# Kernel tuning notes

Measured on AMD Instinct MI355X. Metric: run time of the kernel, lower is better.

The kernel has to match this reference:

```python
import jax, jax.numpy as jnp
import numpy as np

G = 128            # grid_size (hardcoded in NeRFRenderer.__init__)
T = 32             # time_size (reduced from 64 to keep working set < 4GB)
CAS = 1            # cascade = 1 + ceil(log2(bound)), bound = 1
DECAY = 0.95
DENSITY_SCALE = 1.0
DENSITY_THRESH = 0.01


def _expand_bits(v):
    # instant-ngp style 10-bit -> 30-bit expansion (works for 7-bit coords of G=128)
    v = (v * jnp.uint32(0x00010001)) & jnp.uint32(0xFF0000FF)
    v = (v * jnp.uint32(0x00000101)) & jnp.uint32(0x0F00F00F)
    v = (v * jnp.uint32(0x00000011)) & jnp.uint32(0xC30C30C3)
    v = (v * jnp.uint32(0x00000005)) & jnp.uint32(0x49249249)
    return v


def _morton3d(coords):
    # coords: [N, 3] int32 in [0, G)
    x = _expand_bits(coords[:, 0].astype(jnp.uint32))
    y = _expand_bits(coords[:, 1].astype(jnp.uint32))
    z = _expand_bits(coords[:, 2].astype(jnp.uint32))
    return (x | (y << 1) | (z << 2)).astype(jnp.int32)


def setup_inputs() -> dict:
    key = jax.random.key(0)
    k1, k2 = jax.random.split(key)
    density_grid = jax.random.normal(k1, (T, CAS, G ** 3), dtype=jnp.float32) * 0.5
    sigmas = jax.random.uniform(k2, (T, CAS, G ** 3), dtype=jnp.float32)
    return {"density_grid": density_grid, "sigmas": sigmas}


def reference(density_grid, sigmas):
    # full-grid branch of update_extra_state (iter_density < 16)
    g = jnp.arange(G, dtype=jnp.int32)
    xx, yy, zz = jnp.meshgrid(g, g, g, indexing='ij')
    coords = jnp.stack([xx.ravel(), yy.ravel(), zz.ravel()], axis=-1)  # [G^3, 3]
    indices = _morton3d(coords)                                        # [G^3]

    # tmp_grid = -1; tmp_grid[t, cas, indices] = sigmas * density_scale
    tmp_grid = -jnp.ones_like(density_grid)
    tmp_grid = tmp_grid.at[:, :, indices].set(sigmas * DENSITY_SCALE)

    # decay / max merge on mutually-valid cells
    valid = (density_grid >= 0) & (tmp_grid >= 0)
    new_grid = jnp.where(valid, jnp.maximum(density_grid * DECAY, tmp_grid), density_grid)

    # threshold + packbits into bitfield (8 cells per byte, morton order)
    mean_density = jnp.mean(jnp.clip(new_grid, 0.0))
    thresh = jnp.minimum(mean_density, jnp.float32(DENSITY_THRESH))
    bits = (new_grid > thresh).reshape(T, -1, 8)                       # [T, CAS*G^3/8, 8]
    weights = (jnp.int32(1) << jnp.arange(8, dtype=jnp.int32))
    bitfield = jnp.sum(bits.astype(jnp.int32) * weights, axis=-1)      # [T, CAS*G^3/8]
    return new_grid, bitfield
```

## Files before the change

### kernel.cpp

```cpp
#include <hip/hip_runtime.h>

#define G    128
#define G3   (G * G * G)
#define TDIM 32
#define NTOT (TDIM * G3)
#define NBYTES_OUT (NTOT / 8)
#define DECAY 0.95f
#define DTH   0.01f
#define NBLK  (TDIM * 256)

typedef float f32x4 __attribute__((ext_vector_type(4)));
typedef float f32x2 __attribute__((ext_vector_type(2)));

__device__ __forceinline__ unsigned expand3(unsigned v) {
    v = (v * 0x00010001u) & 0xFF0000FFu;
    v = (v * 0x00000101u) & 0x0F00F00Fu;
    v = (v * 0x00000011u) & 0xC30C30C3u;
    v = (v * 0x00000005u) & 0x49249249u;
    return v;
}

__device__ __forceinline__ int swz(int f) {
    return f ^ ((((f >> 11) & 1) << 2) | (((f >> 8) & 1) << 3) | (((f >> 12) & 1) << 4));
}

__device__ __forceinline__ f32x4 merge4(f32x4 v, f32x4 s) {
    f32x4 r;
    r.x = (v.x >= 0.f && s.x >= 0.f) ? fmaxf(v.x * DECAY, s.x) : v.x;
    r.y = (v.y >= 0.f && s.y >= 0.f) ? fmaxf(v.y * DECAY, s.y) : v.y;
    r.z = (v.z >= 0.f && s.z >= 0.f) ? fmaxf(v.z * DECAY, s.z) : v.z;
    r.w = (v.w >= 0.f && s.w >= 0.f) ? fmaxf(v.w * DECAY, s.w) : v.w;
    return r;
}

__global__ __launch_bounds__(512, 8) void
pass1(const float* __restrict__ dg, const float* __restrict__ sg,
      float* __restrict__ out_grid, float* __restrict__ out_bits,
      float* __restrict__ sum_acc)
{
    __shared__ float smem[8192];
    __shared__ float wsum[8];
    const int blk  = blockIdx.x;
    const int t    = blk >> 8;
    const int pp   = blk & 255;
    const int sx   = pp & 15;
    const int sy   = pp >> 4;
    const int base = t * G3;
    const int tid  = threadIdx.x;
    const int w    = tid >> 6;
    const int i    = tid & 63;

    const float* __restrict__ sgt = sg + base + (sx << 17) + (sy << 10);
    f32x4 sa0, sa1, sa2, sa3;
    {
        const int rem = (tid & 255) << 2;
        sa0 = __builtin_nontemporal_load(
                reinterpret_cast<const f32x4*>(sgt + ((tid >> 8) << 14)          + rem));
        sa1 = __builtin_nontemporal_load(
                reinterpret_cast<const f32x4*>(sgt + (((tid + 512) >> 8) << 14)  + rem));
        sa2 = __builtin_nontemporal_load(
                reinterpret_cast<const f32x4*>(sgt + (((tid + 1024) >> 8) << 14) + rem));
        sa3 = __builtin_nontemporal_load(
                reinterpret_cast<const f32x4*>(sgt + (((tid + 1536) >> 8) << 14) + rem));
    }

    const int m_fixed = (int)((expand3((unsigned)sx) << 9) | (expand3((unsigned)sy) << 10));
    const int jgA = base + m_fixed + ((int)expand3((unsigned)w) << 14) + (i << 2);
    const f32x4* dgp = reinterpret_cast<const f32x4*>(dg + jgA);
    const f32x4 v0 = dgp[0];
    const f32x4 v1 = dgp[64];
    const f32x4 v2 = dgp[512];
    const f32x4 v3 = dgp[576];

    {
        const int rem = (tid & 255) << 2;
        *reinterpret_cast<f32x4*>(&smem[swz(((tid >> 8) << 10)          + rem)]) = sa0;
        *reinterpret_cast<f32x4*>(&smem[swz((((tid + 512) >> 8) << 10)  + rem)]) = sa1;
        *reinterpret_cast<f32x4*>(&smem[swz((((tid + 1024) >> 8) << 10) + rem)]) = sa2;
        *reinterpret_cast<f32x4*>(&smem[swz((((tid + 1536) >> 8) << 10) + rem)]) = sa3;
    }
    __syncthreads();

    const int fi = (i & 1) | (((i >> 3) & 1) << 1) | (((i >> 2) & 1) << 8)
                 | (((i >> 5) & 1) << 9) | (((i >> 1) & 1) << 11) | (((i >> 4) & 1) << 12);
    const int S  = (((fi >> 11) & 1) << 2) | (((fi >> 8) & 1) << 3) | (((fi >> 12) & 1) << 4);
    const int A  = w << 4;
    const float* sp0 = &smem[fi | ((A + 0)  ^ S)];
    const float* sp1 = &smem[fi | ((A + 4)  ^ S)];
    const float* sp2 = &smem[fi | ((A + 8)  ^ S)];
    const float* sp3 = &smem[fi | ((A + 12) ^ S)];
    f32x4 s0; s0.x = sp0[0]; s0.y = sp0[1024]; s0.z = sp0[128]; s0.w = sp0[1152];
    f32x4 s1; s1.x = sp1[0]; s1.y = sp1[1024]; s1.z = sp1[128]; s1.w = sp1[1152];
    f32x4 s2; s2.x = sp2[0]; s2.y = sp2[1024]; s2.z = sp2[128]; s2.w = sp2[1152];
    f32x4 s3; s3.x = sp3[0]; s3.y = sp3[1024]; s3.z = sp3[128]; s3.w = sp3[1152];

    const f32x4 r0 = merge4(v0, s0);
    const f32x4 r1 = merge4(v1, s1);
    const f32x4 r2 = merge4(v2, s2);
    const f32x4 r3 = merge4(v3, s3);

    f32x4* ogp = reinterpret_cast<f32x4*>(out_grid + jgA);
    ogp[0]   = r0;
    ogp[64]  = r1;
    ogp[512] = r2;
    ogp[576] = r3;

    float lsum = fmaxf(r0.x, 0.f) + fmaxf(r0.y, 0.f) + fmaxf(r0.z, 0.f) + fmaxf(r0.w, 0.f)
               + fmaxf(r1.x, 0.f) + fmaxf(r1.y, 0.f) + fmaxf(r1.z, 0.f) + fmaxf(r1.w, 0.f)
               + fmaxf(r2.x, 0.f) + fmaxf(r2.y, 0.f) + fmaxf(r2.z, 0.f) + fmaxf(r2.w, 0.f)
               + fmaxf(r3.x, 0.f) + fmaxf(r3.y, 0.f) + fmaxf(r3.z, 0.f) + fmaxf(r3.w, 0.f);

    int n0 = (r0.x > DTH ? 1 : 0) | (r0.y > DTH ? 2 : 0) | (r0.z > DTH ? 4 : 0) | (r0.w > DTH ? 8 : 0);
    int n1 = (r1.x > DTH ? 1 : 0) | (r1.y > DTH ? 2 : 0) | (r1.z > DTH ? 4 : 0) | (r1.w > DTH ? 8 : 0);
    int n2 = (r2.x > DTH ? 1 : 0) | (r2.y > DTH ? 2 : 0) | (r2.z > DTH ? 4 : 0) | (r2.w > DTH ? 8 : 0);
    int n3 = (r3.x > DTH ? 1 : 0) | (r3.y > DTH ? 2 : 0) | (r3.z > DTH ? 4 : 0) | (r3.w > DTH ? 8 : 0);
    const int p0 = __shfl_xor(n0, 1, 64);
    const int p1 = __shfl_xor(n1, 1, 64);
    const int p2 = __shfl_xor(n2, 1, 64);
    const int p3 = __shfl_xor(n3, 1, 64);
    if ((i & 1) == 0) {
        float* bp = out_bits + (jgA >> 3);
        bp[0]   = (float)(n0 | (p0 << 4));
        bp[32]  = (float)(n1 | (p1 << 4));
        bp[256] = (float)(n2 | (p2 << 4));
        bp[288] = (float)(n3 | (p3 << 4));
    }

    #pragma unroll
    for (int offl = 32; offl; offl >>= 1) lsum += __shfl_down(lsum, offl, 64);
    if ((tid & 63) == 0) wsum[tid >> 6] = lsum;
    __syncthreads();
    if (tid == 0) {
        float tot = 0.f;
        #pragma unroll
        for (int k = 0; k < 8; ++k) tot += wsum[k];
        atomicAdd(sum_acc, tot);
    }
}

__global__ __launch_bounds__(256) void
fix_bits(const float* __restrict__ grid, const float* __restrict__ sum_acc,
         float* __restrict__ out_bits)
{
    const float th = fminf(sum_acc[0] / (float)NTOT, DTH);
    if (th == DTH) return;
    for (int n = blockIdx.x * 256 + threadIdx.x; n < NBYTES_OUT; n += 256 * 1024) {
        const float4* g = reinterpret_cast<const float4*>(grid) + (n << 1);
        const float4 a = g[0], b = g[1];
        int byte = (a.x > th ? 1 : 0)   | (a.y > th ? 2 : 0)   |
                   (a.z > th ? 4 : 0)   | (a.w > th ? 8 : 0)   |
                   (b.x > th ? 16 : 0)  | (b.y > th ? 32 : 0)  |
                   (b.z > th ? 64 : 0)  | (b.w > th ? 128 : 0);
        out_bits[n] = (float)byte;
    }
}

extern "C" void kernel_launch(void* const* d_in, const int* in_sizes, int n_in,
                              void* d_out, int out_size, void* d_ws, size_t ws_size,
                              hipStream_t stream)
{
    const float* dg = (const float*)d_in[0];
    const float* sg = (const float*)d_in[1];
    float* out_grid = (float*)d_out;
    float* out_bits = out_grid + NTOT;
    float* sum_acc  = (float*)d_ws;

    hipMemsetAsync(sum_acc, 0, sizeof(float), stream);
    pass1<<<NBLK, 512, 0, stream>>>(dg, sg, out_grid, out_bits, sum_acc);
    fix_bits<<<1024, 256, 0, stream>>>(out_grid, sum_acc, out_bits);
}
```

Baseline: 155.5 us.

## Make shared-memory transpose wave-local and spread sum atomics across eight slots

Each wave now loads the sigma sub-block it will consume itself and transposes it through its own private shared-memory region with a new swizzle. This removes both block-wide barriers. The block-level sum reduction is replaced by one atomic per wave, spread over eight padded accumulators that the fix-up kernel adds together. In exchange there are eight times more atomics and a changed global load pattern for sigmas, with shorter contiguous runs per row.

```diff
diff --git a/kernel.cpp b/kernel.cpp
--- a/kernel.cpp
+++ b/kernel.cpp
@@ -10,7 +10,6 @@
 #define NBLK  (TDIM * 256)
 
 typedef float f32x4 __attribute__((ext_vector_type(4)));
-typedef float f32x2 __attribute__((ext_vector_type(2)));
 
 __device__ __forceinline__ unsigned expand3(unsigned v) {
     v = (v * 0x00010001u) & 0xFF0000FFu;
@@ -18,10 +17,6 @@
     v = (v * 0x00000011u) & 0xC30C30C3u;
     v = (v * 0x00000005u) & 0x49249249u;
     return v;
-}
-
-__device__ __forceinline__ int swz(int f) {
-    return f ^ ((((f >> 11) & 1) << 2) | (((f >> 8) & 1) << 3) | (((f >> 12) & 1) << 4));
 }
 
 __device__ __forceinline__ f32x4 merge4(f32x4 v, f32x4 s) {
@@ -33,13 +28,16 @@
     return r;
 }
 
+__device__ __forceinline__ int lswz(int l) {
+    return l ^ ((((l >> 8) & 1) << 2) | (((l >> 9) & 1) << 3) | (((l >> 6) & 1) << 4));
+}
+
 __global__ __launch_bounds__(512, 8) void
 pass1(const float* __restrict__ dg, const float* __restrict__ sg,
       float* __restrict__ out_grid, float* __restrict__ out_bits,
       float* __restrict__ sum_acc)
 {
     __shared__ float smem[8192];
-    __shared__ float wsum[8];
     const int blk  = blockIdx.x;
     const int t    = blk >> 8;
     const int pp   = blk & 255;
@@ -50,18 +48,23 @@
     const int w    = tid >> 6;
     const int i    = tid & 63;
 
-    const float* __restrict__ sgt = sg + base + (sx << 17) + (sy << 10);
+    const float* __restrict__ sgt = sg + base + (sx << 17) + (sy << 10) + (w << 4);
+    const int lofs = (i & 3) << 2;
+    const int rl   = i >> 2;
     f32x4 sa0, sa1, sa2, sa3;
     {
-        const int rem = (tid & 255) << 2;
+        const int r0 = rl,      x0 = r0 >> 3, y0 = r0 & 7;
+        const int r1 = 16 + rl, x1 = r1 >> 3, y1 = r1 & 7;
+        const int r2 = 32 + rl, x2 = r2 >> 3, y2 = r2 & 7;
+        const int r3 = 48 + rl, x3 = r3 >> 3, y3 = r3 & 7;
         sa0 = __builtin_nontemporal_load(
-                reinterpret_cast<const f32x4*>(sgt + ((tid >> 8) << 14)          + rem));
+                reinterpret_cast<const f32x4*>(sgt + (x0 << 14) + (y0 << 7) + lofs));
         sa1 = __builtin_nontemporal_load(
-                reinterpret_cast<const f32x4*>(sgt + (((tid + 512) >> 8) << 14)  + rem));
+                reinterpret_cast<const f32x4*>(sgt + (x1 << 14) + (y1 << 7) + lofs));
         sa2 = __builtin_nontemporal_load(
-                reinterpret_cast<const f32x4*>(sgt + (((tid + 1024) >> 8) << 14) + rem));
+                reinterpret_cast<const f32x4*>(sgt + (x2 << 14) + (y2 << 7) + lofs));
         sa3 = __builtin_nontemporal_load(
-                reinterpret_cast<const f32x4*>(sgt + (((tid + 1536) >> 8) << 14) + rem));
+                reinterpret_cast<const f32x4*>(sgt + (x3 << 14) + (y3 << 7) + lofs));
     }
 
     const int m_fixed = (int)((expand3((unsigned)sx) << 9) | (expand3((unsigned)sy) << 10));
@@ -72,27 +75,26 @@
     const f32x4 v2 = dgp[512];
     const f32x4 v3 = dgp[576];
 
+    float* const wp = &smem[w << 10];
     {
-        const int rem = (tid & 255) << 2;
-        *reinterpret_cast<f32x4*>(&smem[swz(((tid >> 8) << 10)          + rem)]) = sa0;
-        *reinterpret_cast<f32x4*>(&smem[swz((((tid + 512) >> 8) << 10)  + rem)]) = sa1;
-        *reinterpret_cast<f32x4*>(&smem[swz((((tid + 1024) >> 8) << 10) + rem)]) = sa2;
-        *reinterpret_cast<f32x4*>(&smem[swz((((tid + 1536) >> 8) << 10) + rem)]) = sa3;
+        const int l0 = ((rl)      << 4) + lofs;
+        const int l1 = ((16 + rl) << 4) + lofs;
+        const int l2 = ((32 + rl) << 4) + lofs;
+        const int l3 = ((48 + rl) << 4) + lofs;
+        *reinterpret_cast<f32x4*>(wp + lswz(l0)) = sa0;
+        *reinterpret_cast<f32x4*>(wp + lswz(l1)) = sa1;
+        *reinterpret_cast<f32x4*>(wp + lswz(l2)) = sa2;
+        *reinterpret_cast<f32x4*>(wp + lswz(l3)) = sa3;
     }
-    __syncthreads();
 
-    const int fi = (i & 1) | (((i >> 3) & 1) << 1) | (((i >> 2) & 1) << 8)
-                 | (((i >> 5) & 1) << 9) | (((i >> 1) & 1) << 11) | (((i >> 4) & 1) << 12);
-    const int S  = (((fi >> 11) & 1) << 2) | (((fi >> 8) & 1) << 3) | (((fi >> 12) & 1) << 4);
-    const int A  = w << 4;
-    const float* sp0 = &smem[fi | ((A + 0)  ^ S)];
-    const float* sp1 = &smem[fi | ((A + 4)  ^ S)];
-    const float* sp2 = &smem[fi | ((A + 8)  ^ S)];
-    const float* sp3 = &smem[fi | ((A + 12) ^ S)];
-    f32x4 s0; s0.x = sp0[0]; s0.y = sp0[1024]; s0.z = sp0[128]; s0.w = sp0[1152];
-    f32x4 s1; s1.x = sp1[0]; s1.y = sp1[1024]; s1.z = sp1[128]; s1.w = sp1[1152];
-    f32x4 s2; s2.x = sp2[0]; s2.y = sp2[1024]; s2.z = sp2[128]; s2.w = sp2[1152];
-    f32x4 s3; s3.x = sp3[0]; s3.y = sp3[1024]; s3.z = sp3[128]; s3.w = sp3[1152];
+    const int l0 = (i & 1) | (((i >> 3) & 1) << 1) | (((i >> 2) & 1) << 5)
+                 | (((i >> 5) & 1) << 6) | (((i >> 1) & 1) << 8) | (((i >> 4) & 1) << 9);
+    const int a  = lswz(l0);
+    f32x4 s0, s1, s2, s3;
+    s0.x = wp[a];      s0.y = wp[a ^ 128];      s0.z = wp[a ^ 16];      s0.w = wp[a ^ 144];
+    s1.x = wp[a ^ 4];  s1.y = wp[a ^ 132];      s1.z = wp[a ^ 20];      s1.w = wp[a ^ 148];
+    s2.x = wp[a ^ 8];  s2.y = wp[a ^ 136];      s2.z = wp[a ^ 24];      s2.w = wp[a ^ 152];
+    s3.x = wp[a ^ 12]; s3.y = wp[a ^ 140];      s3.z = wp[a ^ 28];      s3.w = wp[a ^ 156];
 
     const f32x4 r0 = merge4(v0, s0);
     const f32x4 r1 = merge4(v1, s1);
@@ -128,21 +130,17 @@
 
     #pragma unroll
     for (int offl = 32; offl; offl >>= 1) lsum += __shfl_down(lsum, offl, 64);
-    if ((tid & 63) == 0) wsum[tid >> 6] = lsum;
-    __syncthreads();
-    if (tid == 0) {
-        float tot = 0.f;
-        #pragma unroll
-        for (int k = 0; k < 8; ++k) tot += wsum[k];
-        atomicAdd(sum_acc, tot);
-    }
+    if (i == 0) atomicAdd(sum_acc + (w << 5), lsum);
 }
 
 __global__ __launch_bounds__(256) void
 fix_bits(const float* __restrict__ grid, const float* __restrict__ sum_acc,
          float* __restrict__ out_bits)
 {
-    const float th = fminf(sum_acc[0] / (float)NTOT, DTH);
+    float tot = 0.f;
+    #pragma unroll
+    for (int k = 0; k < 8; ++k) tot += sum_acc[k << 5];
+    const float th = fminf(tot / (float)NTOT, DTH);
     if (th == DTH) return;
     for (int n = blockIdx.x * 256 + threadIdx.x; n < NBYTES_OUT; n += 256 * 1024) {
         const float4* g = reinterpret_cast<const float4*>(grid) + (n << 1);
@@ -165,7 +163,7 @@
     float* out_bits = out_grid + NTOT;
     float* sum_acc  = (float*)d_ws;
 
-    hipMemsetAsync(sum_acc, 0, sizeof(float), stream);
+    hipMemsetAsync(sum_acc, 0, 8 * 32 * sizeof(float), stream);
     pass1<<<NBLK, 512, 0, stream>>>(dg, sg, out_grid, out_bits, sum_acc);
     fix_bits<<<1024, 256, 0, stream>>>(out_grid, sum_acc, out_bits);
 }
```

New measurement: 165.2 us. 1.06x slower.
